# Kernel tuning notes

Hardware: AMD Instinct MI355X
Metric: run time of the kernel (lower is better)

Reference implementation:

```python
import jax, jax.numpy as jnp
import numpy as np

SCORE_THRESH = 0.05
NMS_THRESH = 0.5
K = 1000            # max NMS candidates (fixed for jit; padded/masked)
IMG_W, IMG_H = 1333, 800


def setup_inputs() -> dict:
    key = jax.random.key(0)
    k1, k2, k3 = jax.random.split(key, 3)
    N, C = 200000, 81
    class_logits = jax.random.normal(k1, (N, C), dtype=jnp.float32) * 2.0
    # well-formed xyxy boxes inside the image
    cxcy = jax.random.uniform(k2, (N, 2), dtype=jnp.float32) * jnp.array([IMG_W, IMG_H], jnp.float32)
    wh = jax.random.uniform(k3, (N, 2), dtype=jnp.float32) * 200.0 + 1.0
    boxes = jnp.concatenate([cxcy - wh * 0.5, cxcy + wh * 0.5], axis=-1)
    return {"class_logits": class_logits, "boxes": boxes}


def _pairwise_iou(b):
    # b: [K, 4] xyxy -> [K, K]
    area = (b[:, 2] - b[:, 0]) * (b[:, 3] - b[:, 1])
    lt = jnp.maximum(b[:, None, :2], b[None, :, :2])
    rb = jnp.minimum(b[:, None, 2:], b[None, :, 2:])
    wh = jnp.clip(rb - lt, 0.0)
    inter = wh[..., 0] * wh[..., 1]
    return inter / (area[:, None] + area[None, :] - inter + 1e-9)


def reference(class_logits, boxes):
    N, C = class_logits.shape
    prob = jax.nn.softmax(class_logits, axis=-1)            # [N, C]
    # clip_to_image (TO_REMOVE=1 convention: clamp to size-1)
    bx = jnp.stack([
        jnp.clip(boxes[:, 0], 0.0, IMG_W - 1),
        jnp.clip(boxes[:, 1], 0.0, IMG_H - 1),
        jnp.clip(boxes[:, 2], 0.0, IMG_W - 1),
        jnp.clip(boxes[:, 3], 0.0, IMG_H - 1),
    ], axis=-1)                                             # [N, 4]
    flat = prob.reshape(-1)                                 # [N*C], class = idx % C
    idx = jnp.arange(N * C)
    valid = (flat > SCORE_THRESH) & (idx % C != 0)          # fg + score threshold
    masked = jnp.where(valid, flat, -jnp.inf)
    top_scores, top_idx = jax.lax.top_k(masked, K)          # sorted descending
    prop_idx = top_idx // C
    cls = top_idx % C
    bk = bx[prop_idx]                                       # [K, 4]
    valid_k = jnp.isfinite(top_scores)
    scores_k = jnp.where(valid_k, top_scores, 0.0)
    # class-aware greedy NMS over the (sorted) top-K candidates
    conflict = (_pairwise_iou(bk) > NMS_THRESH) & (cls[:, None] == cls[None, :])
    rng = jnp.arange(K)

    def body(i, keep):
        sup = jnp.any(keep & conflict[:, i] & (rng < i))
        return keep.at[i].set(keep[i] & ~sup)

    keep = jax.lax.fori_loop(0, K, body, valid_k)
    out = jnp.concatenate([bk, scores_k[:, None]], axis=-1) * keep[:, None].astype(bk.dtype)
    return out  # [K, 5]: (x1, y1, x2, y2, score), zeroed where suppressed/invalid
```

## Files before the change

kernel.cpp:

```cpp
#include <hip/hip_runtime.h>
#include <stdint.h>
#include <math.h>

#define N_CLS    81
#define TOPK     1000
#define LISTCAP  (1u << 21)
#define CAP2     16384
#define SCORE_TH 0.05f
#define IMG_W    1333.0f
#define IMG_H    800.0f
#define GH_REP   8

#define GH_BASE  1905

#define OFF_CNT    0
#define OFF_CNT2   128
#define OFF_ARRV   256
#define OFF_TICKA  384
#define OFF_TICKB  512
#define OFF_TICKR  640
#define OFF_TICKC  768
#define OFF_PBCA   896
#define OFF_TB     1024
#define OFF_GH     1280
#define OFF_RH     5376
#define MEMSET_BYTES 9472
#define OFF_SEL    16768
#define OFF_SEL2   16793984
#define OFF_BOX    16925056
#define OFF_SCORE  16941056
#define OFF_CLS    16945056
#define OFF_MASK   16949056

#define ROWS_PER_BLK 128
#define TILE_FLOATS  (ROWS_PER_BLK * N_CLS)
#define CBUF_CAP     1024
#define TAIL_BLOCKS  128

typedef unsigned long long u64;

__device__ __forceinline__ void gload_lds16(const float* g, float* l) {
    __builtin_amdgcn_global_load_lds(
        (const __attribute__((address_space(1))) unsigned int*)g,
        (__attribute__((address_space(3))) unsigned int*)l, 16, 0, 0);
}

__device__ __forceinline__ unsigned agent_load_u32(const unsigned* p) {
    return __hip_atomic_load(p, __ATOMIC_RELAXED, __HIP_MEMORY_SCOPE_AGENT);
}
__device__ __forceinline__ u64 agent_load_u64(const u64* p) {
    return __hip_atomic_load(p, __ATOMIC_RELAXED, __HIP_MEMORY_SCOPE_AGENT);
}
__device__ __forceinline__ void agent_store_u32(unsigned* p, unsigned v) {
    __hip_atomic_store(p, v, __ATOMIC_RELAXED, __HIP_MEMORY_SCOPE_AGENT);
}
__device__ __forceinline__ void agent_store_u64(u64* p, u64 v) {
    __hip_atomic_store(p, v, __ATOMIC_RELAXED, __HIP_MEMORY_SCOPE_AGENT);
}
__device__ __forceinline__ void drain_vm() {
    asm volatile("s_waitcnt vmcnt(0)" ::: "memory");
}

__global__ __launch_bounds__(256) void k_pass1(
        const float* __restrict__ logits, int nrows,
        u64* __restrict__ sel, unsigned* __restrict__ cnt,
        unsigned* __restrict__ ghist) {
    __shared__ float tile[TILE_FLOATS];
    __shared__ unsigned lh[128];
    __shared__ u64 cbuf[CBUF_CAP];
    __shared__ unsigned lcnt, gbase;
    int tid = threadIdx.x, wv = tid >> 6, ln = tid & 63;
    for (int i = tid; i < 128; i += 256) lh[i] = 0;
    if (tid == 0) lcnt = 0;

    int base = blockIdx.x * ROWS_PER_BLK;
    int nr = nrows - base; if (nr > ROWS_PER_BLK) nr = ROWS_PER_BLK;
    const float* gtile = logits + (size_t)base * N_CLS;

    if (nr == ROWS_PER_BLK) {
        #pragma unroll
        for (int it = 0; it < 10; ++it) {
            int c = it * 1024 + wv * 256;
            gload_lds16(gtile + c + ln * 4, tile + c);
        }
        if (tid < TILE_FLOATS - 10240) tile[10240 + tid] = gtile[10240 + tid];
    } else {
        for (int i = tid; i < nr * N_CLS; i += 256) tile[i] = gtile[i];
    }
    __syncthreads();

    int r = tid >> 1, h = tid & 1;
    if (r < nr) {
        const int rb = r * N_CLS + h;
        float v[41];
        #pragma unroll
        for (int m = 0; m < 40; ++m) v[m] = tile[rb + 2 * m];
        v[40] = (h == 0) ? tile[rb + 80] : 0.0f;

        float mx = v[0];
        #pragma unroll
        for (int m = 1; m < 40; ++m) mx = fmaxf(mx, v[m]);
        mx = fmaxf(mx, (h == 0) ? v[40] : v[0]);
        float om = __shfl_xor(mx, 1);
        float mrow = fmaxf(mx, om);

        #pragma unroll
        for (int m = 0; m < 40; ++m) v[m] = expf(v[m] - mrow);
        v[40] = (h == 0) ? expf(v[40] - mrow) : 0.0f;

        float stk0 = 0.f, stk1 = 0.f, stk2 = 0.f, stk3 = 0.f, stk4 = 0.f;
        float S = 0.f;
        #pragma unroll
        for (int i = 0; i < 32; ++i) {
            const int b = ((i & 1) << 4) | ((i & 2) << 2) | (i & 4) |
                          ((i & 8) >> 2) | ((i & 16) >> 4);
            float x = v[b];
            if (b < 8) x += v[b + 32];
            else if (b == 8) x = (h == 0) ? x + v[40] : x;
            if (i & 1) { x = stk0 + x;
              if (i & 2) { x = stk1 + x;
                if (i & 4) { x = stk2 + x;
                  if (i & 8) { x = stk3 + x;
                    if (i & 16) { S = stk4 + x; } else stk4 = x;
                  } else stk3 = x;
                } else stk2 = x;
              } else stk1 = x;
            } else stk0 = x;
        }
        float oS = __shfl_xor(S, 1);
        float s = (h == 0) ? (S + oS) : (oS + S);

        float eth = 0.0499f * s;
        unsigned rowflat = (unsigned)(base + r) * N_CLS + (unsigned)h;
        #pragma unroll
        for (int m = 0; m < 41; ++m) {
            float e = v[m];
            if ((m + h) != 0 && e > eth) {
                float p = e / s;
                if (p > SCORE_TH) {
                    unsigned fb = __float_as_uint(p);
                    atomicAdd(&lh[(fb >> 19) - GH_BASE], 1u);
                    u64 key = ((u64)fb << 32) | (u64)(0xFFFFFFu - (rowflat + 2u * (unsigned)m));
                    unsigned pos = atomicAdd(&lcnt, 1u);
                    if (pos < CBUF_CAP) cbuf[pos] = key;
                    else { unsigned gp = atomicAdd(cnt, 1u); if (gp < LISTCAP) sel[gp] = key; }
                }
            }
        }
    }
    __syncthreads();
    unsigned* gh = ghist + (blockIdx.x & (GH_REP - 1)) * 128;
    for (int i = tid; i < 128; i += 256) {
        unsigned vv = lh[i];
        if (vv) atomicAdd(&gh[i], vv);
    }
    unsigned total = lcnt; if (total > CBUF_CAP) total = CBUF_CAP;
    if (tid == 0) gbase = atomicAdd(cnt, total);
    __syncthreads();
    unsigned gb = gbase;
    for (unsigned i = tid; i < total; i += 256) {
        unsigned gp = gb + i;
        if (gp < LISTCAP) sel[gp] = cbuf[i];
    }
}

__global__ __launch_bounds__(1024) void k_tail(
        char* __restrict__ ws, const float* __restrict__ boxes,
        float* __restrict__ out) {
    unsigned* cnt   = (unsigned*)(ws + OFF_CNT);
    unsigned* cnt2  = (unsigned*)(ws + OFF_CNT2);
    unsigned* arrv  = (unsigned*)(ws + OFF_ARRV);
    unsigned* tickA = (unsigned*)(ws + OFF_TICKA);
    unsigned* tickB = (unsigned*)(ws + OFF_TICKB);
    unsigned* tickR = (unsigned*)(ws + OFF_TICKR);
    unsigned* tickC = (unsigned*)(ws + OFF_TICKC);
    u64*      pbca  = (u64*)(ws + OFF_PBCA);
    unsigned* ptb   = (unsigned*)(ws + OFF_TB);
    unsigned* ghist = (unsigned*)(ws + OFF_GH);
    unsigned* rhist = (unsigned*)(ws + OFF_RH);
    u64*      sel   = (u64*)(ws + OFF_SEL);
    u64*      sel2  = (u64*)(ws + OFF_SEL2);
    u64*      boxB  = (u64*)(ws + OFF_BOX);
    unsigned* scrB  = (unsigned*)(ws + OFF_SCORE);
    unsigned* clsB  = (unsigned*)(ws + OFF_CLS);
    u64*      mask  = (u64*)(ws + OFF_MASK);

    __shared__ unsigned scu[1024], sfu[1024];
    __shared__ union {
        unsigned lhist[1024];
        struct { float4 box[TOPK]; int cls[TOPK]; unsigned sc[TOPK]; } c;
    } shu;
    __shared__ u64 words[16];
    __shared__ int schanged, swB;
    __shared__ unsigned swCA, sarr, stk, sfl, stb;
    __shared__ u64 spb;

    int tid = threadIdx.x, ln = tid & 63;
    unsigned nb = gridDim.x;

    if (tid == 0) sarr = atomicAdd(arrv, 1u);
    __syncthreads();
    if (sarr == 0) {
        if (tid < 128) {
            unsigned c = 0;
            #pragma unroll
            for (int rr = 0; rr < GH_REP; ++rr) c += ghist[rr * 128 + tid];
            scu[tid] = c; sfu[tid] = c;
        }
        if (tid == 0) swB = -1;
        __syncthreads();
        #pragma unroll
        for (int off = 1; off < 128; off <<= 1) {
            unsigned a = 0;
            if (tid < 128) a = (tid + off < 128) ? sfu[tid + off] : 0u;
            __syncthreads();
            if (tid < 128) sfu[tid] += a;
            __syncthreads();
        }
        if (tid == 0) swCA = sfu[0];
        __syncthreads();
        if (tid < 128) {
            unsigned incl = sfu[tid], excl = incl - scu[tid];
            if (excl < TOPK && incl >= TOPK) { swB = tid; swCA = excl; }
        }
        __syncthreads();
        if (tid == 0) {
            u64 pk = (1ull << 63) | ((u64)(swCA & 0x3FFu) << 8) | (u64)(unsigned)(swB + 1);
            agent_store_u64(pbca, pk);
        }
    }
    if (tid == 0) {
        u64 v;
        do { __builtin_amdgcn_s_sleep(2); v = agent_load_u64(pbca); } while (!(v >> 63));
        spb = v;
    }
    __syncthreads();
    int B = (int)(unsigned)(spb & 0xFFull) - 1;
    unsigned CA = (unsigned)((spb >> 8) & 0x3FFu);
    unsigned M = *cnt; if (M > LISTCAP) M = LISTCAP;
    unsigned stride = nb * 1024u;
    unsigned tb;

    if (B < 0) {
        tb = 0u;
    } else {
        shu.lhist[tid] = 0;
        __syncthreads();
        unsigned Bbits = (unsigned)(B + GH_BASE);
        for (unsigned i = blockIdx.x * 1024u + tid; i < M; i += stride) {
            unsigned bv = (unsigned)(sel[i] >> 32);
            if ((bv >> 19) == Bbits) atomicAdd(&shu.lhist[(bv >> 9) & 1023u], 1u);
        }
        __syncthreads();
        { unsigned vv = shu.lhist[tid]; if (vv) atomicAdd(&rhist[tid], vv); }
        __syncthreads();
        drain_vm();
        if (tid == 0) stk = atomicAdd(tickA, 1u);
        __syncthreads();
        if (stk == nb - 1) {
            unsigned c = agent_load_u32(&rhist[tid]);
            scu[tid] = c; sfu[tid] = c;
            if (tid == 0) stb = 0;
            __syncthreads();
            #pragma unroll
            for (int off = 1; off < 1024; off <<= 1) {
                unsigned a = (tid + off < 1024) ? sfu[tid + off] : 0u;
                __syncthreads();
                sfu[tid] += a;
                __syncthreads();
            }
            unsigned incl = sfu[tid], excl = incl - scu[tid];
            if (CA + excl < TOPK && CA + incl >= TOPK)
                stb = ((unsigned)(B + GH_BASE) << 19) | ((unsigned)tid << 9);
            __syncthreads();
            if (tid == 0) agent_store_u32(ptb, stb | 0x80000000u);
        }
        if (tid == 0) {
            unsigned f;
            do { __builtin_amdgcn_s_sleep(2); f = agent_load_u32(ptb); } while (!(f >> 31));
            sfl = f;
        }
        __syncthreads();
        tb = sfl & 0x7FFFFFFFu;
    }

    for (unsigned ibase = blockIdx.x * 1024u; ibase < M; ibase += stride) {
        unsigned i = ibase + tid;
        bool act = (i < M);
        u64 key = act ? sel[i] : 0ull;
        bool c = act && ((unsigned)(key >> 32) >= tb);
        u64 b = __ballot(c);
        int n = __popcll(b);
        if (n) {
            unsigned wb = 0;
            if (ln == 0) wb = atomicAdd(cnt2, (unsigned)n);
            wb = __shfl(wb, 0);
            if (c) {
                unsigned pos = wb + (unsigned)__popcll(b & ((1ull << ln) - 1ull));
                if (pos < CAP2) agent_store_u64(&sel2[pos], key);
            }
        }
    }
    __syncthreads();
    drain_vm();
    if (tid == 0) {
        atomicAdd(tickB, 1u);
        unsigned v;
        do { __builtin_amdgcn_s_sleep(2); v = agent_load_u32(tickB); } while (v < nb);
    }
    __syncthreads();

    {
        unsigned S = agent_load_u32(cnt2); if (S > CAP2) S = CAP2;
        unsigned slot = blockIdx.x * 16u + (unsigned)(tid >> 6);
        unsigned nslots = nb * 16u;
        unsigned lim = (S > TOPK) ? S : TOPK;
        for (unsigned k = slot; k < lim; k += nslots) {
            if (k < S) {
                u64 my = agent_load_u64(&sel2[k]);
                unsigned rk = 0;
                for (unsigned j = ln; j < S; j += 64)
                    rk += (agent_load_u64(&sel2[j]) > my) ? 1u : 0u;
                #pragma unroll
                for (int off = 32; off > 0; off >>= 1) rk += __shfl_xor(rk, off);
                if (ln == 0 && rk < TOPK) {
                    float sc = __uint_as_float((unsigned)(my >> 32));
                    unsigned fi = 0xFFFFFFu - (unsigned)(my & 0xFFFFFFFFull);
                    unsigned prop = fi / N_CLS;
                    int cls = (int)(fi - prop * N_CLS);
                    const float* bx = boxes + (size_t)prop * 4;
                    float x1 = fminf(fmaxf(bx[0], 0.0f), IMG_W - 1.0f);
                    float y1 = fminf(fmaxf(bx[1], 0.0f), IMG_H - 1.0f);
                    float x2 = fminf(fmaxf(bx[2], 0.0f), IMG_W - 1.0f);
                    float y2 = fminf(fmaxf(bx[3], 0.0f), IMG_H - 1.0f);
                    agent_store_u64(&boxB[rk * 2],
                        ((u64)__float_as_uint(y1) << 32) | __float_as_uint(x1));
                    agent_store_u64(&boxB[rk * 2 + 1],
                        ((u64)__float_as_uint(y2) << 32) | __float_as_uint(x2));
                    agent_store_u32(&scrB[rk], __float_as_uint(sc));
                    agent_store_u32(&clsB[rk], (unsigned)cls);
                }
            } else if (ln == 0) {
                agent_store_u64(&boxB[k * 2], 0ull);
                agent_store_u64(&boxB[k * 2 + 1], 0ull);
                agent_store_u32(&scrB[k], 0u);
                agent_store_u32(&clsB[k], (unsigned)-1);
            }
        }
    }
    __syncthreads();
    drain_vm();
    if (tid == 0) {
        atomicAdd(tickR, 1u);
        unsigned v;
        do { __builtin_amdgcn_s_sleep(2); v = agent_load_u32(tickR); } while (v < nb);
    }
    __syncthreads();

    if (blockIdx.x >= 16) return;
    if (tid < TOPK) {
        u64 a = agent_load_u64(&boxB[tid * 2]);
        u64 b = agent_load_u64(&boxB[tid * 2 + 1]);
        shu.c.box[tid] = make_float4(
            __uint_as_float((unsigned)a), __uint_as_float((unsigned)(a >> 32)),
            __uint_as_float((unsigned)b), __uint_as_float((unsigned)(b >> 32)));
        shu.c.cls[tid] = (int)agent_load_u32(&clsB[tid]);
        shu.c.sc[tid]  = agent_load_u32(&scrB[tid]);
    }
    __syncthreads();
    {
        int t = blockIdx.x * 1024 + tid;
        int i = t >> 4, w = t & 15;
        if (i < TOPK) {
            float4 bi = shu.c.box[i];
            int ci = shu.c.cls[i];
            float ai = (bi.z - bi.x) * (bi.w - bi.y);
            u64 m = 0;
            int jbase = w << 6;
            for (int jj = 0; jj < 64; jj++) {
                int j = jbase + jj;
                if (j >= TOPK) break;
                float4 bj = shu.c.box[j];
                float aj = (bj.z - bj.x) * (bj.w - bj.y);
                float ww = fmaxf(fminf(bi.z, bj.z) - fmaxf(bi.x, bj.x), 0.0f);
                float hh = fmaxf(fminf(bi.w, bj.w) - fmaxf(bi.y, bj.y), 0.0f);
                float inter = ww * hh;
                float iou = inter / (ai + aj - inter + 1e-9f);
                if (iou > 0.5f && ci == shu.c.cls[j]) m |= (1ull << jj);
            }
            agent_store_u64(&mask[(size_t)i * 16 + w], m);
        }
    }
    __syncthreads();
    drain_vm();
    if (tid == 0) stk = atomicAdd(tickC, 1u);
    __syncthreads();
    if (stk != 15u) return;

    int wv = tid >> 6;
    bool valid = (tid < TOPK) && (__uint_as_float(shu.c.sc[tid]) > 0.0f);
    u64 row[16];
    #pragma unroll
    for (int w = 0; w < 16; w++)
        row[w] = (tid < TOPK) ? agent_load_u64(&mask[(size_t)tid * 16 + w]) : 0ull;
    u64 lowmask = (1ull << ln) - 1ull;
    bool keep = valid;
    for (int it = 0; it < 1024; ++it) {
        u64 b = __ballot(keep);
        if (ln == 0) words[wv] = b;
        if (tid == 0) schanged = 0;
        __syncthreads();
        u64 sup = 0;
        for (int w = 0; w <= wv; w++) {
            u64 kw = words[w];
            if (w == wv) kw &= lowmask;
            sup |= row[w] & kw;
        }
        bool nk = valid && (sup == 0ull);
        if (nk != keep) schanged = 1;
        keep = nk;
        __syncthreads();
        if (!schanged) break;
    }
    if (tid < TOPK) {
        float4 bx = shu.c.box[tid];
        float sc = __uint_as_float(shu.c.sc[tid]);
        out[tid * 5 + 0] = keep ? bx.x : 0.0f;
        out[tid * 5 + 1] = keep ? bx.y : 0.0f;
        out[tid * 5 + 2] = keep ? bx.z : 0.0f;
        out[tid * 5 + 3] = keep ? bx.w : 0.0f;
        out[tid * 5 + 4] = keep ? sc : 0.0f;
    }
}

extern "C" void kernel_launch(void* const* d_in, const int* in_sizes, int n_in,
                              void* d_out, int out_size, void* d_ws, size_t ws_size,
                              hipStream_t stream) {
    const float* logits = (const float*)d_in[0];
    const float* boxes  = (const float*)d_in[1];
    float* out = (float*)d_out;
    int nrows = in_sizes[0] / N_CLS;

    char* w = (char*)d_ws;
    unsigned* cnt   = (unsigned*)(w + OFF_CNT);
    unsigned* ghist = (unsigned*)(w + OFF_GH);
    u64* sel        = (u64*)(w + OFF_SEL);

    hipMemsetAsync(w, 0, MEMSET_BYTES, stream);

    int nblk = (nrows + ROWS_PER_BLK - 1) / ROWS_PER_BLK;
    k_pass1<<<nblk, 256, 0, stream>>>(logits, nrows, sel, cnt, ghist);
    k_tail<<<TAIL_BLOCKS, 1024, 0, stream>>>(w, boxes, out);
}
```

Measured before the change: 200.0 us.

## Fuse refine histogram into compaction pass and pad LDS box layout

Merges the second-level histogram pass with the candidate compaction pass, so the selection list is read once instead of twice. Candidates are compacted at the coarse bucket threshold and finer-threshold entries are skipped during ranking, which removes one grid-wide barrier (tickB). The LDS box storage also changes from float4 AoS to padded SoA arrays to reduce bank conflicts in the IoU mask computation. In exchange, more entries may land in sel2 (bounded by CAP2) and the ranking loop scans a larger S.

```diff
diff --git a/kernel.cpp b/kernel.cpp
--- a/kernel.cpp
+++ b/kernel.cpp
@@ -17,7 +17,6 @@
 #define OFF_CNT2   128
 #define OFF_ARRV   256
 #define OFF_TICKA  384
-#define OFF_TICKB  512
 #define OFF_TICKR  640
 #define OFF_TICKC  768
 #define OFF_PBCA   896
@@ -36,8 +35,11 @@
 #define TILE_FLOATS  (ROWS_PER_BLK * N_CLS)
 #define CBUF_CAP     1024
 #define TAIL_BLOCKS  128
+#define PADK         1016
 
 typedef unsigned long long u64;
+
+__device__ __forceinline__ int ipad(int j) { return j + (j >> 6); }
 
 __device__ __forceinline__ void gload_lds16(const float* g, float* l) {
     __builtin_amdgcn_global_load_lds(
@@ -171,7 +173,6 @@
     unsigned* cnt2  = (unsigned*)(ws + OFF_CNT2);
     unsigned* arrv  = (unsigned*)(ws + OFF_ARRV);
     unsigned* tickA = (unsigned*)(ws + OFF_TICKA);
-    unsigned* tickB = (unsigned*)(ws + OFF_TICKB);
     unsigned* tickR = (unsigned*)(ws + OFF_TICKR);
     unsigned* tickC = (unsigned*)(ws + OFF_TICKC);
     u64*      pbca  = (u64*)(ws + OFF_PBCA);
@@ -188,7 +189,10 @@
     __shared__ unsigned scu[1024], sfu[1024];
     __shared__ union {
         unsigned lhist[1024];
-        struct { float4 box[TOPK]; int cls[TOPK]; unsigned sc[TOPK]; } c;
+        struct {
+            float x1[PADK], y1[PADK], x2[PADK], y2[PADK];
+            int cls[PADK]; unsigned sc[PADK];
+        } c;
     } shu;
     __shared__ u64 words[16];
     __shared__ int schanged, swB;
@@ -239,56 +243,19 @@
     unsigned CA = (unsigned)((spb >> 8) & 0x3FFu);
     unsigned M = *cnt; if (M > LISTCAP) M = LISTCAP;
     unsigned stride = nb * 1024u;
-    unsigned tb;
-
-    if (B < 0) {
-        tb = 0u;
-    } else {
-        shu.lhist[tid] = 0;
-        __syncthreads();
-        unsigned Bbits = (unsigned)(B + GH_BASE);
-        for (unsigned i = blockIdx.x * 1024u + tid; i < M; i += stride) {
-            unsigned bv = (unsigned)(sel[i] >> 32);
-            if ((bv >> 19) == Bbits) atomicAdd(&shu.lhist[(bv >> 9) & 1023u], 1u);
-        }
-        __syncthreads();
-        { unsigned vv = shu.lhist[tid]; if (vv) atomicAdd(&rhist[tid], vv); }
-        __syncthreads();
-        drain_vm();
-        if (tid == 0) stk = atomicAdd(tickA, 1u);
-        __syncthreads();
-        if (stk == nb - 1) {
-            unsigned c = agent_load_u32(&rhist[tid]);
-            scu[tid] = c; sfu[tid] = c;
-            if (tid == 0) stb = 0;
-            __syncthreads();
-            #pragma unroll
-            for (int off = 1; off < 1024; off <<= 1) {
-                unsigned a = (tid + off < 1024) ? sfu[tid + off] : 0u;
-                __syncthreads();
-                sfu[tid] += a;
-                __syncthreads();
-            }
-            unsigned incl = sfu[tid], excl = incl - scu[tid];
-            if (CA + excl < TOPK && CA + incl >= TOPK)
-                stb = ((unsigned)(B + GH_BASE) << 19) | ((unsigned)tid << 9);
-            __syncthreads();
-            if (tid == 0) agent_store_u32(ptb, stb | 0x80000000u);
-        }
-        if (tid == 0) {
-            unsigned f;
-            do { __builtin_amdgcn_s_sleep(2); f = agent_load_u32(ptb); } while (!(f >> 31));
-            sfl = f;
-        }
-        __syncthreads();
-        tb = sfl & 0x7FFFFFFFu;
-    }
-
+    unsigned tbc = (B < 0) ? 0u : ((unsigned)(B + GH_BASE) << 19);
+    unsigned Bbits = (unsigned)(B + GH_BASE);
+
+    shu.lhist[tid] = 0;
+    __syncthreads();
     for (unsigned ibase = blockIdx.x * 1024u; ibase < M; ibase += stride) {
         unsigned i = ibase + tid;
         bool act = (i < M);
         u64 key = act ? sel[i] : 0ull;
-        bool c = act && ((unsigned)(key >> 32) >= tb);
+        unsigned bv = (unsigned)(key >> 32);
+        if (act && B >= 0 && (bv >> 19) == Bbits)
+            atomicAdd(&shu.lhist[(bv >> 9) & 1023u], 1u);
+        bool c = act && (bv >= tbc) && (B >= 0 || true) && (key != 0ull);
         u64 b = __ballot(c);
         int n = __popcll(b);
         if (n) {
@@ -302,13 +269,36 @@
         }
     }
     __syncthreads();
+    { unsigned vv = shu.lhist[tid]; if (vv) atomicAdd(&rhist[tid], vv); }
+    __syncthreads();
     drain_vm();
+    if (tid == 0) stk = atomicAdd(tickA, 1u);
+    __syncthreads();
+    if (stk == nb - 1) {
+        unsigned c = agent_load_u32(&rhist[tid]);
+        scu[tid] = c; sfu[tid] = c;
+        if (tid == 0) stb = 0;
+        __syncthreads();
+        #pragma unroll
+        for (int off = 1; off < 1024; off <<= 1) {
+            unsigned a = (tid + off < 1024) ? sfu[tid + off] : 0u;
+            __syncthreads();
+            sfu[tid] += a;
+            __syncthreads();
+        }
+        unsigned incl = sfu[tid], excl = incl - scu[tid];
+        if (B >= 0 && CA + excl < TOPK && CA + incl >= TOPK)
+            stb = ((unsigned)(B + GH_BASE) << 19) | ((unsigned)tid << 9);
+        __syncthreads();
+        if (tid == 0) agent_store_u32(ptb, stb | 0x80000000u);
+    }
     if (tid == 0) {
-        atomicAdd(tickB, 1u);
-        unsigned v;
-        do { __builtin_amdgcn_s_sleep(2); v = agent_load_u32(tickB); } while (v < nb);
-    }
-    __syncthreads();
+        unsigned f;
+        do { __builtin_amdgcn_s_sleep(2); f = agent_load_u32(ptb); } while (!(f >> 31));
+        sfl = f;
+    }
+    __syncthreads();
+    unsigned tb = sfl & 0x7FFFFFFFu;
 
     {
         unsigned S = agent_load_u32(cnt2); if (S > CAP2) S = CAP2;
@@ -318,6 +308,7 @@
         for (unsigned k = slot; k < lim; k += nslots) {
             if (k < S) {
                 u64 my = agent_load_u64(&sel2[k]);
+                if ((unsigned)(my >> 32) < tb) continue;
                 unsigned rk = 0;
                 for (unsigned j = ln; j < S; j += 64)
                     rk += (agent_load_u64(&sel2[j]) > my) ? 1u : 0u;
@@ -350,43 +341,50 @@
     }
     __syncthreads();
     drain_vm();
+    if (tid == 0) stk = atomicAdd(tickR, 1u);
+    __syncthreads();
+    if (blockIdx.x >= 16) return;
     if (tid == 0) {
-        atomicAdd(tickR, 1u);
         unsigned v;
         do { __builtin_amdgcn_s_sleep(2); v = agent_load_u32(tickR); } while (v < nb);
     }
     __syncthreads();
 
-    if (blockIdx.x >= 16) return;
     if (tid < TOPK) {
         u64 a = agent_load_u64(&boxB[tid * 2]);
         u64 b = agent_load_u64(&boxB[tid * 2 + 1]);
-        shu.c.box[tid] = make_float4(
-            __uint_as_float((unsigned)a), __uint_as_float((unsigned)(a >> 32)),
-            __uint_as_float((unsigned)b), __uint_as_float((unsigned)(b >> 32)));
-        shu.c.cls[tid] = (int)agent_load_u32(&clsB[tid]);
-        shu.c.sc[tid]  = agent_load_u32(&scrB[tid]);
+        int ip = ipad(tid);
+        shu.c.x1[ip] = __uint_as_float((unsigned)a);
+        shu.c.y1[ip] = __uint_as_float((unsigned)(a >> 32));
+        shu.c.x2[ip] = __uint_as_float((unsigned)b);
+        shu.c.y2[ip] = __uint_as_float((unsigned)(b >> 32));
+        shu.c.cls[ip] = (int)agent_load_u32(&clsB[tid]);
+        shu.c.sc[ip]  = agent_load_u32(&scrB[tid]);
     }
     __syncthreads();
     {
         int t = blockIdx.x * 1024 + tid;
         int i = t >> 4, w = t & 15;
         if (i < TOPK) {
-            float4 bi = shu.c.box[i];
-            int ci = shu.c.cls[i];
-            float ai = (bi.z - bi.x) * (bi.w - bi.y);
+            int ip = ipad(i);
+            float x1 = shu.c.x1[ip], y1 = shu.c.y1[ip];
+            float x2 = shu.c.x2[ip], y2 = shu.c.y2[ip];
+            int ci = shu.c.cls[ip];
+            float ai = (x2 - x1) * (y2 - y1);
             u64 m = 0;
             int jbase = w << 6;
             for (int jj = 0; jj < 64; jj++) {
                 int j = jbase + jj;
                 if (j >= TOPK) break;
-                float4 bj = shu.c.box[j];
-                float aj = (bj.z - bj.x) * (bj.w - bj.y);
-                float ww = fmaxf(fminf(bi.z, bj.z) - fmaxf(bi.x, bj.x), 0.0f);
-                float hh = fmaxf(fminf(bi.w, bj.w) - fmaxf(bi.y, bj.y), 0.0f);
+                int jp = ipad(j);
+                float u1 = shu.c.x1[jp], w1 = shu.c.y1[jp];
+                float u2 = shu.c.x2[jp], w2 = shu.c.y2[jp];
+                float aj = (u2 - u1) * (w2 - w1);
+                float ww = fmaxf(fminf(x2, u2) - fmaxf(x1, u1), 0.0f);
+                float hh = fmaxf(fminf(y2, w2) - fmaxf(y1, w1), 0.0f);
                 float inter = ww * hh;
                 float iou = inter / (ai + aj - inter + 1e-9f);
-                if (iou > 0.5f && ci == shu.c.cls[j]) m |= (1ull << jj);
+                if (iou > 0.5f && ci == shu.c.cls[jp]) m |= (1ull << jj);
             }
             agent_store_u64(&mask[(size_t)i * 16 + w], m);
         }
@@ -398,7 +396,8 @@
     if (stk != 15u) return;
 
     int wv = tid >> 6;
-    bool valid = (tid < TOPK) && (__uint_as_float(shu.c.sc[tid]) > 0.0f);
+    int myip = ipad(tid < TOPK ? tid : 0);
+    bool valid = (tid < TOPK) && (__uint_as_float(shu.c.sc[myip]) > 0.0f);
     u64 row[16];
     #pragma unroll
     for (int w = 0; w < 16; w++)
@@ -423,12 +422,11 @@
         if (!schanged) break;
     }
     if (tid < TOPK) {
-        float4 bx = shu.c.box[tid];
-        float sc = __uint_as_float(shu.c.sc[tid]);
-        out[tid * 5 + 0] = keep ? bx.x : 0.0f;
-        out[tid * 5 + 1] = keep ? bx.y : 0.0f;
-        out[tid * 5 + 2] = keep ? bx.z : 0.0f;
-        out[tid * 5 + 3] = keep ? bx.w : 0.0f;
+        float sc = __uint_as_float(shu.c.sc[myip]);
+        out[tid * 5 + 0] = keep ? shu.c.x1[myip] : 0.0f;
+        out[tid * 5 + 1] = keep ? shu.c.y1[myip] : 0.0f;
+        out[tid * 5 + 2] = keep ? shu.c.x2[myip] : 0.0f;
+        out[tid * 5 + 3] = keep ? shu.c.y2[myip] : 0.0f;
         out[tid * 5 + 4] = keep ? sc : 0.0f;
     }
 }
```

Result: faster. 186.1 us (-6.9%).
